# Performance work log

Hardware: AMD Instinct MI355X
Metric: run time of the kernel (lower is better)

The kernel has to match this reference:

```python
import jax, jax.numpy as jnp
import numpy as np

EPS = 1e-6
NUM_HEADS = 32
HEAD_DIM = 128


def _rms_norm(x, w):
    # RMSNorm over last dim (head_dim)
    var = jnp.mean(x * x, axis=-1, keepdims=True)
    return x * jax.lax.rsqrt(var + EPS) * w


def _rotate_half(x):
    x1, x2 = jnp.split(x, 2, axis=-1)
    return jnp.concatenate([-x2, x1], axis=-1)


def _apply_rope(x, cos, sin):
    # x: [b, t, h, d]; cos/sin: [t, d] -> broadcast over batch and heads
    c = cos[None, :, None, :]
    s = sin[None, :, None, :]
    return x * c + _rotate_half(x) * s


def setup_inputs() -> dict:
    key = jax.random.key(0)
    ks = jax.random.split(key, 7)
    b, q_len, ctx_len, hidden = 4, 64, 4096, 4096
    total = ctx_len + q_len
    return {
        "hidden_states": jax.random.normal(ks[0], (b, q_len, hidden), jnp.float32),
        "target_hidden": jax.random.normal(ks[1], (b, ctx_len, hidden), jnp.float32),
        "cos": jax.random.uniform(ks[2], (total, HEAD_DIM), jnp.float32, -1.0, 1.0),
        "sin": jax.random.uniform(ks[3], (total, HEAD_DIM), jnp.float32, -1.0, 1.0),
        "Wqkv": jax.random.normal(ks[4], (hidden, 3 * hidden), jnp.float32) * 0.02,
        "Wo": jax.random.normal(ks[5], (hidden, hidden), jnp.float32) * 0.02,
        "q_norm_w": jnp.ones((HEAD_DIM,), jnp.float32),
    }


def reference(hidden_states, target_hidden, cos, sin, Wqkv, Wo, q_norm_w):
    b, q_len, hidden = hidden_states.shape
    ctx_len = target_hidden.shape[1]
    H, D = NUM_HEADS, HEAD_DIM

    # fused QKV projection; only the query slice is consumed (per source)
    qkv = jnp.einsum("bqh,hz->bqz", hidden_states, Wqkv)
    q = qkv[..., : H * D].reshape(b, q_len, H, D)

    # q_norm is applied twice in the source forward
    q = _rms_norm(_rms_norm(q, q_norm_w), q_norm_w)

    # KV built by concatenating raw target_hidden context with draft hidden states
    kv = jnp.concatenate([target_hidden, hidden_states], axis=1)  # [b, ctx+q, hidden]
    k = kv.reshape(b, ctx_len + q_len, H, D)
    v = k  # v = k view per source (rope applied only to k)

    # rotary: draft queries occupy positions ctx_len .. ctx_len+q_len-1
    q = _apply_rope(q, cos[ctx_len:], sin[ctx_len:])
    k = _apply_rope(k, cos, sin)

    # attention (full attention of draft queries over context + draft keys)
    scale = 1.0 / jnp.sqrt(jnp.asarray(D, q.dtype))
    scores = jnp.einsum("bqhd,bkhd->bhqk", q, k) * scale
    probs = jax.nn.softmax(scores, axis=-1)
    out = jnp.einsum("bhqk,bkhd->bqhd", probs, v)

    out = out.reshape(b, q_len, H * D)
    return jnp.einsum("bqh,ho->bqo", out, Wo)
```

## Files before the change

### kernel.cpp

```cpp
#include <hip/hip_runtime.h>

typedef __attribute__((ext_vector_type(8))) short bf16x8;
typedef __attribute__((ext_vector_type(4))) float f32x4;
typedef __attribute__((ext_vector_type(4))) short s16x4;

#define DEV __device__ __forceinline__

DEV short f2bf(float f) {
  union { float f; unsigned u; } v; v.f = f;
  unsigned r = v.u + 0x7fffu + ((v.u >> 16) & 1u);
  return (short)(r >> 16);
}

__global__ __launch_bounds__(256) void transpose_to_bf16(
    const float* __restrict__ in, long ld, short* __restrict__ out, int K) {
  __shared__ short tile[64][66];
  long k0 = blockIdx.x * 64L, n0 = blockIdx.y * 64L;
  int t = threadIdx.x;
  {
    int kl = t >> 4, nl4 = (t & 15) * 4;
#pragma unroll
    for (int i = 0; i < 4; i++) {
      int k = kl + i * 16;
      float4 v = *(const float4*)(in + (k0 + k) * ld + n0 + nl4);
      s16x4 w; w.x = f2bf(v.x); w.y = f2bf(v.y); w.z = f2bf(v.z); w.w = f2bf(v.w);
      *(s16x4*)&tile[k][nl4] = w;
    }
  }
  __syncthreads();
  {
    int nl = t >> 4, kl4 = (t & 15) * 4;
#pragma unroll
    for (int i = 0; i < 4; i++) {
      int n = nl + i * 16;
      s16x4 w;
      w.x = tile[kl4 + 0][n]; w.y = tile[kl4 + 1][n];
      w.z = tile[kl4 + 2][n]; w.w = tile[kl4 + 3][n];
      *(s16x4*)(out + (n0 + n) * (long)K + k0 + kl4) = w;
    }
  }
}

template <bool AF32>
__global__ __launch_bounds__(256) void gemm_bt(
    const void* __restrict__ Ap, const short* __restrict__ Bt,
    float* __restrict__ C, int N, int K) {
  __shared__ short As[8 * 544];
  __shared__ short Bs[8 * 544];
  int t = threadIdx.x;
  long m0 = blockIdx.y * 64L, n0 = blockIdx.x * 64L;
  int lane = t & 63, quad = lane >> 4, m16 = lane & 15;
  int wave = t >> 6, wm = wave & 1, wn = wave >> 1;
  f32x4 acc[2][2] = {};
  int r = t >> 3, c = t & 7;

  for (int k0 = 0; k0 < K; k0 += 64) {
    __syncthreads();
#pragma unroll
    for (int half = 0; half < 2; half++) {
      int rr = r + half * 32;
      int fb = (c >> 2) * 4 + (rr >> 4);
      int pos = (c & 3) * 16 + (rr & 15);
      int off = fb * 544 + pos * 8 + (pos >> 4) * 8;
      bf16x8 av;
      if (AF32) {
        const float* src = (const float*)Ap + (m0 + rr) * (long)K + k0 + c * 8;
        float4 x = *(const float4*)src;
        float4 y = *(const float4*)(src + 4);
        av[0] = f2bf(x.x); av[1] = f2bf(x.y); av[2] = f2bf(x.z); av[3] = f2bf(x.w);
        av[4] = f2bf(y.x); av[5] = f2bf(y.y); av[6] = f2bf(y.z); av[7] = f2bf(y.w);
      } else {
        av = *(const bf16x8*)((const short*)Ap + (m0 + rr) * (long)K + k0 + c * 8);
      }
      *(bf16x8*)&As[off] = av;
      *(bf16x8*)&Bs[off] = *(const bf16x8*)(Bt + (n0 + rr) * (long)K + k0 + c * 8);
    }
    __syncthreads();
#pragma unroll
    for (int s = 0; s < 2; s++) {
      int lo = lane * 8 + quad * 8;
      bf16x8 a0 = *(bf16x8*)&As[(s * 4 + wm * 2 + 0) * 544 + lo];
      bf16x8 a1 = *(bf16x8*)&As[(s * 4 + wm * 2 + 1) * 544 + lo];
      bf16x8 b0 = *(bf16x8*)&Bs[(s * 4 + wn * 2 + 0) * 544 + lo];
      bf16x8 b1 = *(bf16x8*)&Bs[(s * 4 + wn * 2 + 1) * 544 + lo];
      acc[0][0] = __builtin_amdgcn_mfma_f32_16x16x32_bf16(a0, b0, acc[0][0], 0, 0, 0);
      acc[0][1] = __builtin_amdgcn_mfma_f32_16x16x32_bf16(a0, b1, acc[0][1], 0, 0, 0);
      acc[1][0] = __builtin_amdgcn_mfma_f32_16x16x32_bf16(a1, b0, acc[1][0], 0, 0, 0);
      acc[1][1] = __builtin_amdgcn_mfma_f32_16x16x32_bf16(a1, b1, acc[1][1], 0, 0, 0);
    }
  }
#pragma unroll
  for (int i = 0; i < 2; i++)
#pragma unroll
    for (int j = 0; j < 2; j++)
#pragma unroll
      for (int rg = 0; rg < 4; rg++) {
        long m = m0 + (wm * 2 + i) * 16 + quad * 4 + rg;
        long n = n0 + (wn * 2 + j) * 16 + m16;
        C[m * (long)N + n] = acc[i][j][rg];
      }
}

__global__ __launch_bounds__(256) void q_norm_rope(
    const float* __restrict__ qtmp, const float* __restrict__ qw,
    const float* __restrict__ cosp, const float* __restrict__ sinp,
    short* __restrict__ qr) {
  int wid = blockIdx.x * 4 + (threadIdx.x >> 6);
  int lane = threadIdx.x & 63;
  int rrow = wid >> 5, h = wid & 31;
  long base = (long)rrow * 4096 + h * 128;
  float x1 = qtmp[base + lane], x2 = qtmp[base + 64 + lane];
  float w1 = qw[lane], w2 = qw[64 + lane];
  float ss = x1 * x1 + x2 * x2;
#pragma unroll
  for (int m = 1; m < 64; m <<= 1) ss += __shfl_xor(ss, m, 64);
  float rs = rsqrtf(ss * (1.0f / 128.0f) + 1e-6f);
  float y1 = x1 * rs * w1, y2 = x2 * rs * w2;
  float ss2 = y1 * y1 + y2 * y2;
#pragma unroll
  for (int m = 1; m < 64; m <<= 1) ss2 += __shfl_xor(ss2, m, 64);
  float rs2 = rsqrtf(ss2 * (1.0f / 128.0f) + 1e-6f);
  float z1 = y1 * rs2 * w1, z2 = y2 * rs2 * w2;
  long cpos = (long)(4096 + (rrow & 63)) * 128;
  float c1 = cosp[cpos + lane], c2 = cosp[cpos + 64 + lane];
  float s1 = sinp[cpos + lane], s2 = sinp[cpos + 64 + lane];
  const float scale = 0.08838834764831845f;
  float o1 = (z1 * c1 - z2 * s1) * scale;
  float o2 = (z2 * c2 + z1 * s2) * scale;
  qr[base + lane] = f2bf(o1);
  qr[base + 64 + lane] = f2bf(o2);
}

#define ATT_SPLIT 5
#define ATT_LKV 832
#define ATT_TILES 13

__global__ __launch_bounds__(256) void attn_kernel(
    const short* __restrict__ qr, const float* __restrict__ th,
    const float* __restrict__ hs, const float* __restrict__ cosp,
    const float* __restrict__ sinp, float* __restrict__ part,
    float* __restrict__ mstat, float* __restrict__ lstat) {
  __shared__ short Ks[64 * 136];
  __shared__ short Vt[128 * 80];
  __shared__ short Ps[64 * 72];
  int bh = blockIdx.x, split = blockIdx.y;
  int b = bh >> 5, h = bh & 31;
  int t = threadIdx.x;
  int wave = t >> 6, lane = t & 63, quad = lane >> 4, m16 = lane & 15;

  bf16x8 aq[4];
  {
    const short* qrow = qr + (long)(b * 64 + wave * 16 + m16) * 4096 + h * 128;
#pragma unroll
    for (int s = 0; s < 4; s++) aq[s] = *(const bf16x8*)(qrow + s * 32 + quad * 8);
  }
  float mi[4] = {-INFINITY, -INFINITY, -INFINITY, -INFINITY};
  float li[4] = {0.f, 0.f, 0.f, 0.f};
  f32x4 oacc[8] = {};

  int srow = t >> 2;
  int sc = t & 3;

  for (int tile = 0; tile < ATT_TILES; tile++) {
    int l0 = split * ATT_LKV + tile * 64;
    __syncthreads();
    {
      int lg = l0 + srow;
      const float* kvrow = (lg < 4096)
          ? th + ((long)b * 4096 + lg) * 4096 + h * 128
          : hs + ((long)b * 64 + (lg - 4096)) * 4096 + h * 128;
      const float* crow = cosp + (long)lg * 128;
      const float* srw = sinp + (long)lg * 128;
#pragma unroll
      for (int i = 0; i < 2; i++) {
        int c = sc + 4 * i;
        int d1 = c * 8, d2 = d1 + 64;
        alignas(16) float xa[8], xb[8], cA[8], sA[8], cB[8], sB[8];
        *(float4*)&xa[0] = *(const float4*)(kvrow + d1);
        *(float4*)&xa[4] = *(const float4*)(kvrow + d1 + 4);
        *(float4*)&xb[0] = *(const float4*)(kvrow + d2);
        *(float4*)&xb[4] = *(const float4*)(kvrow + d2 + 4);
        *(float4*)&cA[0] = *(const float4*)(crow + d1);
        *(float4*)&cA[4] = *(const float4*)(crow + d1 + 4);
        *(float4*)&cB[0] = *(const float4*)(crow + d2);
        *(float4*)&cB[4] = *(const float4*)(crow + d2 + 4);
        *(float4*)&sA[0] = *(const float4*)(srw + d1);
        *(float4*)&sA[4] = *(const float4*)(srw + d1 + 4);
        *(float4*)&sB[0] = *(const float4*)(srw + d2);
        *(float4*)&sB[4] = *(const float4*)(srw + d2 + 4);
        bf16x8 k1, k2, v1, v2;
#pragma unroll
        for (int j = 0; j < 8; j++) {
          k1[j] = f2bf(xa[j] * cA[j] - xb[j] * sA[j]);
          k2[j] = f2bf(xb[j] * cB[j] + xa[j] * sB[j]);
          v1[j] = f2bf(xa[j]);
          v2[j] = f2bf(xb[j]);
        }
        *(bf16x8*)&Ks[srow * 136 + d1] = k1;
        *(bf16x8*)&Ks[srow * 136 + d2] = k2;
#pragma unroll
        for (int j = 0; j < 8; j++) {
          Vt[(d1 + j) * 80 + srow] = v1[j];
          Vt[(d2 + j) * 80 + srow] = v2[j];
        }
      }
    }
    __syncthreads();

    f32x4 sacc[4] = {};
#pragma unroll
    for (int s = 0; s < 4; s++)
#pragma unroll
      for (int nt = 0; nt < 4; nt++) {
        bf16x8 bk = *(const bf16x8*)&Ks[(nt * 16 + m16) * 136 + s * 32 + quad * 8];
        sacc[nt] = __builtin_amdgcn_mfma_f32_16x16x32_bf16(aq[s], bk, sacc[nt], 0, 0, 0);
      }

    float mnew[4], alpha[4];
#pragma unroll
    for (int rg = 0; rg < 4; rg++) {
      float mx = fmaxf(fmaxf(sacc[0][rg], sacc[1][rg]), fmaxf(sacc[2][rg], sacc[3][rg]));
#pragma unroll
      for (int msk = 1; msk < 16; msk <<= 1) mx = fmaxf(mx, __shfl_xor(mx, msk, 16));
      mnew[rg] = fmaxf(mi[rg], mx);
      alpha[rg] = __expf(mi[rg] - mnew[rg]);
      mi[rg] = mnew[rg];
    }
#pragma unroll
    for (int rg = 0; rg < 4; rg++) {
      float rs = 0.f;
#pragma unroll
      for (int nt = 0; nt < 4; nt++) {
        float p = __expf(sacc[nt][rg] - mnew[rg]);
        rs += p;
        Ps[(wave * 16 + quad * 4 + rg) * 72 + nt * 16 + m16] = f2bf(p);
      }
#pragma unroll
      for (int msk = 1; msk < 16; msk <<= 1) rs += __shfl_xor(rs, msk, 16);
      li[rg] = li[rg] * alpha[rg] + rs;
    }
#pragma unroll
    for (int nt = 0; nt < 8; nt++) {
      f32x4 o = oacc[nt];
      o[0] *= alpha[0]; o[1] *= alpha[1]; o[2] *= alpha[2]; o[3] *= alpha[3];
      oacc[nt] = o;
    }

    bf16x8 ap[2];
#pragma unroll
    for (int s = 0; s < 2; s++)
      ap[s] = *(const bf16x8*)&Ps[(wave * 16 + m16) * 72 + s * 32 + quad * 8];
#pragma unroll
    for (int s = 0; s < 2; s++)
#pragma unroll
      for (int nt = 0; nt < 8; nt++) {
        bf16x8 bv = *(const bf16x8*)&Vt[(nt * 16 + m16) * 80 + s * 32 + quad * 8];
        oacc[nt] = __builtin_amdgcn_mfma_f32_16x16x32_bf16(ap[s], bv, oacc[nt], 0, 0, 0);
      }
  }

  long pbase = (long)(bh * ATT_SPLIT + split) * 64;
#pragma unroll
  for (int nt = 0; nt < 8; nt++)
#pragma unroll
    for (int rg = 0; rg < 4; rg++)
      part[(pbase + wave * 16 + quad * 4 + rg) * 128 + nt * 16 + m16] = oacc[nt][rg];
  if (m16 == 0)
#pragma unroll
    for (int rg = 0; rg < 4; rg++) {
      mstat[pbase + wave * 16 + quad * 4 + rg] = mi[rg];
      lstat[pbase + wave * 16 + quad * 4 + rg] = li[rg];
    }
}

__global__ __launch_bounds__(128) void attn_merge(
    const float* __restrict__ part, const float* __restrict__ mstat,
    const float* __restrict__ lstat, short* __restrict__ attn) {
  int idx = blockIdx.x;
  int bh = idx >> 6, q = idx & 63;
  int d = threadIdx.x;
  float m5[ATT_SPLIT], l5[ATT_SPLIT];
  float mstar = -INFINITY;
#pragma unroll
  for (int s = 0; s < ATT_SPLIT; s++) {
    m5[s] = mstat[((long)bh * ATT_SPLIT + s) * 64 + q];
    l5[s] = lstat[((long)bh * ATT_SPLIT + s) * 64 + q];
    mstar = fmaxf(mstar, m5[s]);
  }
  float denom = 0.f, o = 0.f;
#pragma unroll
  for (int s = 0; s < ATT_SPLIT; s++) {
    float w = __expf(m5[s] - mstar);
    denom += w * l5[s];
    o += w * part[(((long)bh * ATT_SPLIT + s) * 64 + q) * 128 + d];
  }
  int b = bh >> 5, h = bh & 31;
  attn[(long)(b * 64 + q) * 4096 + h * 128 + d] = f2bf(o / denom);
}

extern "C" void kernel_launch(void* const* d_in, const int* in_sizes, int n_in,
                              void* d_out, int out_size, void* d_ws, size_t ws_size,
                              hipStream_t stream) {
  const float* hs = (const float*)d_in[0];
  const float* th = (const float*)d_in[1];
  const float* cosp = (const float*)d_in[2];
  const float* sinp = (const float*)d_in[3];
  const float* wqkv = (const float*)d_in[4];
  const float* wo = (const float*)d_in[5];
  const float* qw = (const float*)d_in[6];
  float* out = (float*)d_out;

  char* ws = (char*)d_ws;
  short* WT = (short*)ws;
  float* qtmp = (float*)(ws + (32L << 20));
  short* qrb = (short*)(ws + (36L << 20));
  short* attn = (short*)(ws + (38L << 20));
  float* part = (float*)(ws + (40L << 20));
  float* mstat = (float*)(ws + (60L << 20));
  float* lstat = (float*)(ws + (61L << 20));

  transpose_to_bf16<<<dim3(64, 64), 256, 0, stream>>>(wqkv, 12288, WT, 4096);
  gemm_bt<true><<<dim3(64, 4), 256, 0, stream>>>(hs, WT, qtmp, 4096, 4096);
  q_norm_rope<<<2048, 256, 0, stream>>>(qtmp, qw, cosp, sinp, qrb);
  attn_kernel<<<dim3(128, ATT_SPLIT), 256, 0, stream>>>(qrb, th, hs, cosp, sinp,
                                                        part, mstat, lstat);
  attn_merge<<<128 * 64, 128, 0, stream>>>(part, mstat, lstat, attn);
  transpose_to_bf16<<<dim3(64, 64), 256, 0, stream>>>(wo, 4096, WT, 4096);
  gemm_bt<false><<<dim3(64, 4), 256, 0, stream>>>(attn, WT, out, 4096, 4096);
}
```

Baseline: 725.7 us.

## Split-K the projection GEMMs and raise attention KV split count

Both 256x4096x4096 GEMMs are split four ways along K, giving 1024 blocks instead of 256 so more of the many CUs are occupied. The Q partials are summed inside q_norm_rope, and the output partials are summed by a new reduce4 kernel. Attention KV splits go from 5 to 13 for the same reason, and the merge kernel is changed to handle the larger split count. In exchange the code writes and reads extra partial buffers and adds one more kernel launch.

```diff
diff --git a/kernel.cpp b/kernel.cpp
--- a/kernel.cpp
+++ b/kernel.cpp
@@ -42,19 +42,21 @@
 }
 
 template <bool AF32>
-__global__ __launch_bounds__(256) void gemm_bt(
+__global__ __launch_bounds__(256) void gemm_bt_split(
     const void* __restrict__ Ap, const short* __restrict__ Bt,
-    float* __restrict__ C, int N, int K) {
+    float* __restrict__ Cp, int M, int N, int K, int Kc) {
   __shared__ short As[8 * 544];
   __shared__ short Bs[8 * 544];
   int t = threadIdx.x;
   long m0 = blockIdx.y * 64L, n0 = blockIdx.x * 64L;
+  int z = blockIdx.z;
   int lane = t & 63, quad = lane >> 4, m16 = lane & 15;
   int wave = t >> 6, wm = wave & 1, wn = wave >> 1;
   f32x4 acc[2][2] = {};
   int r = t >> 3, c = t & 7;
 
-  for (int k0 = 0; k0 < K; k0 += 64) {
+  int kbeg = z * Kc, kend = kbeg + Kc;
+  for (int k0 = kbeg; k0 < kend; k0 += 64) {
     __syncthreads();
 #pragma unroll
     for (int half = 0; half < 2; half++) {
@@ -89,6 +91,7 @@
       acc[1][1] = __builtin_amdgcn_mfma_f32_16x16x32_bf16(a1, b1, acc[1][1], 0, 0, 0);
     }
   }
+  float* C = Cp + (long)z * M * N;
 #pragma unroll
   for (int i = 0; i < 2; i++)
 #pragma unroll
@@ -99,6 +102,22 @@
         long n = n0 + (wn * 2 + j) * 16 + m16;
         C[m * (long)N + n] = acc[i][j][rg];
       }
+}
+
+__global__ __launch_bounds__(256) void reduce4(
+    const float* __restrict__ p, float* __restrict__ out, long n4, long stride) {
+  long i = (blockIdx.x * 256L + threadIdx.x);
+  if (i >= n4) return;
+  float4 a = *(const float4*)(p + i * 4);
+  float4 b = *(const float4*)(p + stride + i * 4);
+  float4 c = *(const float4*)(p + 2 * stride + i * 4);
+  float4 d = *(const float4*)(p + 3 * stride + i * 4);
+  float4 r;
+  r.x = a.x + b.x + c.x + d.x;
+  r.y = a.y + b.y + c.y + d.y;
+  r.z = a.z + b.z + c.z + d.z;
+  r.w = a.w + b.w + c.w + d.w;
+  *(float4*)(out + i * 4) = r;
 }
 
 __global__ __launch_bounds__(256) void q_norm_rope(
@@ -109,7 +128,11 @@
   int lane = threadIdx.x & 63;
   int rrow = wid >> 5, h = wid & 31;
   long base = (long)rrow * 4096 + h * 128;
-  float x1 = qtmp[base + lane], x2 = qtmp[base + 64 + lane];
+  const long STR = 256L * 4096;
+  float x1 = qtmp[base + lane] + qtmp[STR + base + lane] +
+             qtmp[2 * STR + base + lane] + qtmp[3 * STR + base + lane];
+  float x2 = qtmp[base + 64 + lane] + qtmp[STR + base + 64 + lane] +
+             qtmp[2 * STR + base + 64 + lane] + qtmp[3 * STR + base + 64 + lane];
   float w1 = qw[lane], w2 = qw[64 + lane];
   float ss = x1 * x1 + x2 * x2;
 #pragma unroll
@@ -131,9 +154,9 @@
   qr[base + 64 + lane] = f2bf(o2);
 }
 
-#define ATT_SPLIT 5
-#define ATT_LKV 832
-#define ATT_TILES 13
+#define ATT_SPLIT 13
+#define ATT_LKV 320
+#define ATT_TILES 5
 
 __global__ __launch_bounds__(256) void attn_kernel(
     const short* __restrict__ qr, const float* __restrict__ th,
@@ -279,20 +302,17 @@
   int idx = blockIdx.x;
   int bh = idx >> 6, q = idx & 63;
   int d = threadIdx.x;
-  float m5[ATT_SPLIT], l5[ATT_SPLIT];
   float mstar = -INFINITY;
 #pragma unroll
+  for (int s = 0; s < ATT_SPLIT; s++)
+    mstar = fmaxf(mstar, mstat[((long)bh * ATT_SPLIT + s) * 64 + q]);
+  float denom = 0.f, o = 0.f;
+#pragma unroll
   for (int s = 0; s < ATT_SPLIT; s++) {
-    m5[s] = mstat[((long)bh * ATT_SPLIT + s) * 64 + q];
-    l5[s] = lstat[((long)bh * ATT_SPLIT + s) * 64 + q];
-    mstar = fmaxf(mstar, m5[s]);
-  }
-  float denom = 0.f, o = 0.f;
-#pragma unroll
-  for (int s = 0; s < ATT_SPLIT; s++) {
-    float w = __expf(m5[s] - mstar);
-    denom += w * l5[s];
-    o += w * part[(((long)bh * ATT_SPLIT + s) * 64 + q) * 128 + d];
+    long sq = ((long)bh * ATT_SPLIT + s) * 64 + q;
+    float w = __expf(mstat[sq] - mstar);
+    denom += w * lstat[sq];
+    o += w * part[sq * 128 + d];
   }
   int b = bh >> 5, h = bh & 31;
   attn[(long)(b * 64 + q) * 4096 + h * 128 + d] = f2bf(o / denom);
@@ -313,18 +333,20 @@
   char* ws = (char*)d_ws;
   short* WT = (short*)ws;
   float* qtmp = (float*)(ws + (32L << 20));
-  short* qrb = (short*)(ws + (36L << 20));
-  short* attn = (short*)(ws + (38L << 20));
-  float* part = (float*)(ws + (40L << 20));
-  float* mstat = (float*)(ws + (60L << 20));
-  float* lstat = (float*)(ws + (61L << 20));
+  short* qrb = (short*)(ws + (48L << 20));
+  short* attn = (short*)(ws + (50L << 20));
+  float* part = (float*)(ws + (52L << 20));
+  float* mstat = (float*)(ws + (108L << 20));
+  float* lstat = (float*)(ws + (109L << 20));
+  float* otmp = (float*)(ws + (110L << 20));
 
   transpose_to_bf16<<<dim3(64, 64), 256, 0, stream>>>(wqkv, 12288, WT, 4096);
-  gemm_bt<true><<<dim3(64, 4), 256, 0, stream>>>(hs, WT, qtmp, 4096, 4096);
+  gemm_bt_split<true><<<dim3(64, 4, 4), 256, 0, stream>>>(hs, WT, qtmp, 256, 4096, 4096, 1024);
   q_norm_rope<<<2048, 256, 0, stream>>>(qtmp, qw, cosp, sinp, qrb);
   attn_kernel<<<dim3(128, ATT_SPLIT), 256, 0, stream>>>(qrb, th, hs, cosp, sinp,
                                                         part, mstat, lstat);
   attn_merge<<<128 * 64, 128, 0, stream>>>(part, mstat, lstat, attn);
   transpose_to_bf16<<<dim3(64, 64), 256, 0, stream>>>(wo, 4096, WT, 4096);
-  gemm_bt<false><<<dim3(64, 4), 256, 0, stream>>>(attn, WT, out, 4096, 4096);
-}
+  gemm_bt_split<false><<<dim3(64, 4, 4), 256, 0, stream>>>(attn, WT, otmp, 256, 4096, 4096, 1024);
+  reduce4<<<1024, 256, 0, stream>>>(otmp, out, 262144, 1L << 20);
+}
```

After: 636.1 us. 12.4% less time.
